# Kernel optimization log

Measured on AMD Instinct MI355X. Metric: run time of the kernel, lower is better.

Reference implementation:

```python
import jax, jax.numpy as jnp
import numpy as np

D_MODEL = 2048
N_HEADS = 32
N_KV_HEADS = 8
HEAD_DIM = D_MODEL // N_HEADS  # 64
N_REP = N_HEADS // N_KV_HEADS  # 4
SCALE = HEAD_DIM ** -0.5


def _rope_tables(seq_len):
    inv_freq = 1.0 / (10000.0 ** (jnp.arange(0, HEAD_DIM, 2, dtype=jnp.float32) / HEAD_DIM))
    t = jnp.arange(seq_len, dtype=jnp.float32)
    freqs = jnp.outer(t, inv_freq)  # [S, HEAD_DIM/2]
    return jnp.cos(freqs), jnp.sin(freqs)


def _apply_rope(x, cos, sin):
    # x: [b, h, s, d]; interleaved even/odd rotation, matching torch stack+flatten
    x_r, x_i = x[..., ::2], x[..., 1::2]
    out_r = x_r * cos - x_i * sin
    out_i = x_r * sin + x_i * cos
    out = jnp.stack([out_r, out_i], axis=-1)  # [b,h,s,d/2,2]
    return out.reshape(x.shape)


def setup_inputs() -> dict:
    key = jax.random.key(0)
    ks = jax.random.split(key, 5)
    bs, seq_len = 2, 2048
    std = D_MODEL ** -0.5
    x = jax.random.normal(ks[0], (bs, seq_len, D_MODEL), dtype=jnp.float32)
    wq = jax.random.normal(ks[1], (N_HEADS * HEAD_DIM, D_MODEL), dtype=jnp.float32) * std
    wk = jax.random.normal(ks[2], (N_KV_HEADS * HEAD_DIM, D_MODEL), dtype=jnp.float32) * std
    wv = jax.random.normal(ks[3], (N_KV_HEADS * HEAD_DIM, D_MODEL), dtype=jnp.float32) * std
    wo = jax.random.normal(ks[4], (D_MODEL, N_HEADS * HEAD_DIM), dtype=jnp.float32) * std
    return {"x": x, "wq": wq, "wk": wk, "wv": wv, "wo": wo}


def reference(x, wq, wk, wv, wo):
    bs, seq_len, _ = x.shape
    # fused-style QKV projections (nn.Linear: x @ W.T)
    q = (x @ wq.T).reshape(bs, seq_len, N_HEADS, HEAD_DIM).transpose(0, 2, 1, 3)
    k = (x @ wk.T).reshape(bs, seq_len, N_KV_HEADS, HEAD_DIM).transpose(0, 2, 1, 3)
    v = (x @ wv.T).reshape(bs, seq_len, N_KV_HEADS, HEAD_DIM).transpose(0, 2, 1, 3)
    cos, sin = _rope_tables(seq_len)  # [S, HEAD_DIM/2], broadcast over b,h
    q = _apply_rope(q, cos, sin)
    k = _apply_rope(k, cos, sin)
    # GQA: repeat KV heads to match Q heads
    k = jnp.repeat(k, N_REP, axis=1)  # [b, H, s, d]
    v = jnp.repeat(v, N_REP, axis=1)
    attn = jnp.einsum('bhqd,bhkd->bhqk', q, k) * SCALE
    causal = jnp.triu(jnp.ones((seq_len, seq_len), dtype=bool), k=1)
    attn = jnp.where(causal, -jnp.inf, attn)
    attn = jax.nn.softmax(attn, axis=-1)
    out = jnp.einsum('bhqk,bhkd->bhqd', attn, v)
    out = out.transpose(0, 2, 1, 3).reshape(bs, seq_len, D_MODEL)
    return out @ wo.T
```

## Files before the change

kernel.cpp:

```cpp
#include <hip/hip_runtime.h>

#define SEQ    2048
#define DM     2048
#define QKVN   3072
#define VTR    64

typedef short s16x8 __attribute__((ext_vector_type(8)));
typedef float f32x4 __attribute__((ext_vector_type(4)));
typedef float f32x16 __attribute__((ext_vector_type(16)));
typedef unsigned u32x4 __attribute__((ext_vector_type(4)));
typedef unsigned short us;

#define MFMA(a,b,c)   __builtin_amdgcn_mfma_f32_16x16x32_bf16((a),(b),(c),0,0,0)
#define MFMA32(a,b,c) __builtin_amdgcn_mfma_f32_32x32x16_bf16((a),(b),(c),0,0,0)

__device__ __forceinline__ float bf2f(us u) {
    unsigned v = ((unsigned)u) << 16;
    return __builtin_bit_cast(float, v);
}
__device__ __forceinline__ us f2bf(float f) {
    unsigned u = __builtin_bit_cast(unsigned, f);
    u += 0x7FFFu + ((u >> 16) & 1u);
    return (us)(u >> 16);
}
__device__ __forceinline__ unsigned cvtpk(float lo, float hi) {
    unsigned r;
    asm("v_cvt_pk_bf16_f32 %0, %1, %2" : "=v"(r) : "v"(lo), "v"(hi));
    return r;
}
__device__ __forceinline__ void glds16(const us* g, us* l) {
    __builtin_amdgcn_global_load_lds((__attribute__((address_space(1))) void*)g,
                                     (__attribute__((address_space(3))) void*)l, 16, 0, 0);
}

__global__ __launch_bounds__(256) void cvt_all(const float* __restrict__ x,
                                               const float* __restrict__ wq,
                                               const float* __restrict__ wk,
                                               const float* __restrict__ wv,
                                               const float* __restrict__ wo,
                                               us* __restrict__ xb,
                                               us* __restrict__ wdst) {
    int i = (blockIdx.x * blockDim.x + threadIdx.x) * 2;
    const float* src;
    int off;
    if (i < 2097152)      { src = x;  off = 0; }
    else {
        int j = i - 2097152;
        if (j < 1048576)      { src = wq; off = 2097152; }
        else if (j < 1310720) { src = wk; off = 2097152 + 1048576; }
        else if (j < 1572864) { src = wv; off = 2097152 + 1310720; }
        else                  { src = wo; off = 2097152 + 1572864; }
    }
    const int base = i - off;
    float4 v0 = ((const float4*)src)[base];
    float4 v1 = ((const float4*)src)[base + 1];
    s16x8 o;
    o[0] = (short)f2bf(v0.x); o[1] = (short)f2bf(v0.y);
    o[2] = (short)f2bf(v0.z); o[3] = (short)f2bf(v0.w);
    o[4] = (short)f2bf(v1.x); o[5] = (short)f2bf(v1.y);
    o[6] = (short)f2bf(v1.z); o[7] = (short)f2bf(v1.w);
    us* d = (i < 2097152) ? xb : wdst;
    const int di = (i < 2097152) ? i : i - 2097152;
    *(s16x8*)(d + di * 4) = o;
}

template <typename OutT, bool ROPE>
__global__ __launch_bounds__(512) void gemm_bt2(const us* __restrict__ A, const us* __restrict__ W,
                                                OutT* __restrict__ C, us* __restrict__ vt,
                                                int M, int N, int K) {
    __shared__ us lA[2][2][128 * 64];
    __shared__ us lB[2][2][128 * 64];
    const int tid = threadIdx.x, lane = tid & 63, wave = tid >> 6;
    const int quad = lane >> 4, lr = lane & 15;
    const int mh = wave >> 2;
    const int wnx = wave & 3;
    const int bh = wnx >> 1, br0 = (wnx & 1) * 64;
    const int m0 = blockIdx.x * 256, n0 = blockIdx.y * 256;

    const int srow = tid >> 3;
    const int scol = ((tid & 7) ^ (srow & 7)) * 8;
    const int sdst = srow * 64 + (tid & 7) * 8;

    const us* gA = A + (size_t)m0 * K;
    const us* gB = W + (size_t)n0 * K;

    auto stageH = [&](int s) {
        const int t = s >> 2, ty = s & 3, par = t & 1;
        const us* src;
        us* dst;
        if (ty < 2) { src = gA + (size_t)(ty * 128) * K;       dst = &lA[par][ty][0]; }
        else        { src = gB + (size_t)((ty - 2) * 128) * K; dst = &lB[par][ty - 2][0]; }
        src += t * 64;
        glds16(src + (size_t)srow * K + scol,        dst + sdst);
        glds16(src + (size_t)(srow + 64) * K + scol, dst + sdst + 64 * 64);
    };

    const int rsw = (lr & 7) << 3;
    auto rdA = [&](int par, int kk, int i) {
        return *(const s16x8*)&lA[par][mh][(i * 16 + lr) * 64 + ((kk * 32 + quad * 8) ^ rsw)];
    };
    auto rdB = [&](int par, int kk, int j) {
        return *(const s16x8*)&lB[par][bh][(br0 + j * 16 + lr) * 64 + ((kk * 32 + quad * 8) ^ rsw)];
    };

    f32x4 acc[8][4] = {};
    const int NT = K / 64;

    stageH(0); stageH(1); stageH(2); stageH(3); stageH(4);
    asm volatile("s_waitcnt vmcnt(2)" ::: "memory");
    __builtin_amdgcn_s_barrier();

    s16x8 af[2][4], ag[2][4], bfr[2][2], bg[2][2];
    for (int t = 0; t < NT; ++t) {
        const int par = t & 1;
#pragma unroll
        for (int kk = 0; kk < 2; kk++) {
#pragma unroll
            for (int i = 0; i < 4; i++) af[kk][i] = rdA(par, kk, i);
#pragma unroll
            for (int j = 0; j < 2; j++) bfr[kk][j] = rdB(par, kk, j);
        }
        if (t + 1 < NT) stageH(4 * (t + 1) + 1);
        __builtin_amdgcn_s_barrier();
        asm volatile("s_waitcnt lgkmcnt(0)" ::: "memory");
        __builtin_amdgcn_s_setprio(1);
#pragma unroll
        for (int i = 0; i < 4; i++)
#pragma unroll
            for (int j = 0; j < 2; j++)
#pragma unroll
                for (int kk = 0; kk < 2; kk++)
                    acc[i][j] = MFMA(af[kk][i], bfr[kk][j], acc[i][j]);
        __builtin_amdgcn_s_setprio(0);
        __builtin_amdgcn_s_barrier();
#pragma unroll
        for (int kk = 0; kk < 2; kk++)
#pragma unroll
            for (int j = 0; j < 2; j++) bg[kk][j] = rdB(par, kk, 2 + j);
        if (t + 1 < NT) stageH(4 * (t + 1) + 2);
        __builtin_amdgcn_s_barrier();
        asm volatile("s_waitcnt lgkmcnt(0)" ::: "memory");
        __builtin_amdgcn_s_setprio(1);
#pragma unroll
        for (int i = 0; i < 4; i++)
#pragma unroll
            for (int j = 0; j < 2; j++)
#pragma unroll
                for (int kk = 0; kk < 2; kk++)
                    acc[i][2 + j] = MFMA(af[kk][i], bg[kk][j], acc[i][2 + j]);
        __builtin_amdgcn_s_setprio(0);
        __builtin_amdgcn_s_barrier();
#pragma unroll
        for (int kk = 0; kk < 2; kk++)
#pragma unroll
            for (int i = 0; i < 4; i++) ag[kk][i] = rdA(par, kk, 4 + i);
        if (t + 1 < NT) stageH(4 * (t + 1) + 3);
        __builtin_amdgcn_s_barrier();
        asm volatile("s_waitcnt lgkmcnt(0)" ::: "memory");
        __builtin_amdgcn_s_setprio(1);
#pragma unroll
        for (int i = 0; i < 4; i++)
#pragma unroll
            for (int j = 0; j < 2; j++)
#pragma unroll
                for (int kk = 0; kk < 2; kk++)
                    acc[4 + i][j] = MFMA(ag[kk][i], bfr[kk][j], acc[4 + i][j]);
        __builtin_amdgcn_s_setprio(0);
        __builtin_amdgcn_s_barrier();
        if (t + 2 < NT) stageH(4 * (t + 2));
        __builtin_amdgcn_s_setprio(1);
#pragma unroll
        for (int i = 0; i < 4; i++)
#pragma unroll
            for (int j = 0; j < 2; j++)
#pragma unroll
                for (int kk = 0; kk < 2; kk++)
                    acc[4 + i][2 + j] = MFMA(ag[kk][i], bg[kk][j], acc[4 + i][2 + j]);
        __builtin_amdgcn_s_setprio(0);
        if (t + 1 < NT) {
            if (t + 2 < NT) asm volatile("s_waitcnt vmcnt(2)" ::: "memory");
            else            asm volatile("s_waitcnt vmcnt(0)" ::: "memory");
            __builtin_amdgcn_s_barrier();
        }
    }

    const bool vblk = ROPE && (n0 >= 2560);
#pragma unroll
    for (int i = 0; i < 8; i++)
#pragma unroll
        for (int j = 0; j < 4; j++) {
            const int row0 = m0 + mh * 128 + i * 16 + quad * 4;
            const int col  = n0 + wnx * 64 + j * 16 + lr;
            if (vblk) {
                const int d = col - 2560;
                const int b = row0 >> 11, s = row0 & (SEQ - 1);
                ushort4 o4;
                o4.x = f2bf(acc[i][j][0]); o4.y = f2bf(acc[i][j][1]);
                o4.z = f2bf(acc[i][j][2]); o4.w = f2bf(acc[i][j][3]);
                *(ushort4*)(vt + ((size_t)b * 512 + d) * SEQ + s) = o4;
            } else {
#pragma unroll
                for (int r = 0; r < 4; r++) {
                    const int row = row0 + r;
                    float v = acc[i][j][r];
                    if (ROPE && n0 < 2560) {
                        int pair = (col >> 1) & 31;
                        float inv = exp2f((float)pair * (-13.2877124f / 32.0f));
                        float ang = (float)(row & (SEQ - 1)) * inv;
                        float c = __cosf(ang), sn = __sinf(ang);
                        float p = __shfl_xor(v, 1);
                        v = v * c + ((col & 1) ? p * sn : -p * sn);
                    }
                    if constexpr (sizeof(OutT) == 2)
                        C[(size_t)row * N + col] = f2bf(v);
                    else
                        C[(size_t)row * N + col] = v;
                }
            }
        }
}

template <typename OutT>
__global__ __launch_bounds__(512) void gemm_bt2n(const us* __restrict__ A, const us* __restrict__ W,
                                                 OutT* __restrict__ C, int M, int N, int K) {
    __shared__ us lA[2][2][128 * 64];
    __shared__ us lB[2][128 * 64];
    const int tid = threadIdx.x, lane = tid & 63, wave = tid >> 6;
    const int quad = lane >> 4, lr = lane & 15;
    const int mh = wave >> 2;
    const int wnx = wave & 3;
    const int m0 = blockIdx.x * 256, n0 = blockIdx.y * 128;

    const int srow = tid >> 3;
    const int scol = ((tid & 7) ^ (srow & 7)) * 8;
    const int sdst = srow * 64 + (tid & 7) * 8;

    const us* gA = A + (size_t)m0 * K;
    const us* gB = W + (size_t)n0 * K;

    auto stageH = [&](int t, int ty) {
        const int par = t & 1;
        const us* src;
        us* dst;
        if (ty < 2) { src = gA + (size_t)(ty * 128) * K; dst = &lA[par][ty][0]; }
        else        { src = gB;                           dst = &lB[par][0]; }
        src += t * 64;
        glds16(src + (size_t)srow * K + scol,        dst + sdst);
        glds16(src + (size_t)(srow + 64) * K + scol, dst + sdst + 64 * 64);
    };

    const int rsw = (lr & 7) << 3;
    auto rdA = [&](int par, int kk, int i) {
        return *(const s16x8*)&lA[par][mh][(i * 16 + lr) * 64 + ((kk * 32 + quad * 8) ^ rsw)];
    };
    auto rdB = [&](int par, int kk, int j) {
        return *(const s16x8*)&lB[par][(wnx * 32 + j * 16 + lr) * 64 + ((kk * 32 + quad * 8) ^ rsw)];
    };

    f32x4 acc[8][2] = {};
    const int NT = K / 64;

    stageH(0, 0); stageH(0, 1); stageH(0, 2); stageH(1, 0);
    asm volatile("s_waitcnt vmcnt(2)" ::: "memory");
    __builtin_amdgcn_s_barrier();

    s16x8 af[2][4], ag[2][4], bfr[2][2];
    for (int t = 0; t < NT; ++t) {
        const int par = t & 1;
#pragma unroll
        for (int kk = 0; kk < 2; kk++) {
#pragma unroll
            for (int i = 0; i < 4; i++) af[kk][i] = rdA(par, kk, i);
#pragma unroll
            for (int j = 0; j < 2; j++) bfr[kk][j] = rdB(par, kk, j);
        }
        if (t + 1 < NT) stageH(t + 1, 1);
        __builtin_amdgcn_s_barrier();
        asm volatile("s_waitcnt lgkmcnt(0)" ::: "memory");
        __builtin_amdgcn_s_setprio(1);
#pragma unroll
        for (int i = 0; i < 4; i++)
#pragma unroll
            for (int j = 0; j < 2; j++)
#pragma unroll
                for (int kk = 0; kk < 2; kk++)
                    acc[i][j] = MFMA(af[kk][i], bfr[kk][j], acc[i][j]);
        __builtin_amdgcn_s_setprio(0);
        __builtin_amdgcn_s_barrier();
#pragma unroll
        for (int kk = 0; kk < 2; kk++)
#pragma unroll
            for (int i = 0; i < 4; i++) ag[kk][i] = rdA(par, kk, 4 + i);
        if (t + 1 < NT) stageH(t + 1, 2);
        __builtin_amdgcn_s_barrier();
        asm volatile("s_waitcnt lgkmcnt(0)" ::: "memory");
        __builtin_amdgcn_s_setprio(1);
#pragma unroll
        for (int i = 0; i < 4; i++)
#pragma unroll
            for (int j = 0; j < 2; j++)
#pragma unroll
                for (int kk = 0; kk < 2; kk++)
                    acc[4 + i][j] = MFMA(ag[kk][i], bfr[kk][j], acc[4 + i][j]);
        __builtin_amdgcn_s_setprio(0);
        if (t + 2 < NT) stageH(t + 2, 0);
        if (t + 1 < NT) {
            if (t + 2 < NT) asm volatile("s_waitcnt vmcnt(2)" ::: "memory");
            else            asm volatile("s_waitcnt vmcnt(0)" ::: "memory");
            __builtin_amdgcn_s_barrier();
        }
    }

#pragma unroll
    for (int i = 0; i < 8; i++)
#pragma unroll
        for (int j = 0; j < 2; j++)
#pragma unroll
            for (int r = 0; r < 4; r++) {
                int row = m0 + mh * 128 + i * 16 + quad * 4 + r;
                int col = n0 + wnx * 32 + j * 16 + lr;
                if constexpr (sizeof(OutT) == 2)
                    C[(size_t)row * N + col] = f2bf(acc[i][j][r]);
                else
                    C[(size_t)row * N + col] = acc[i][j][r];
            }
}

__global__ __launch_bounds__(256, 2) void flash_attn(const us* __restrict__ qkv,
                                                     const us* __restrict__ vt,
                                                     us* __restrict__ o) {
    const int bh = blockIdx.y, b = bh >> 5, h = bh & 31, kvh = h >> 2;
    const int wave = threadIdx.x >> 6, lane = threadIdx.x & 63;
    const int half = lane >> 5, l5 = lane & 31;
    const int jb = ((int)blockIdx.x + (int)(blockIdx.y >> 3)) & 7;
    const int j = jb * 4 + wave;
    const int q00 = j * 32, q01 = (63 - j) * 32;
    const int kbm0 = j, kbm1 = 63 - j;
    const us* kbase = qkv + (size_t)b * SEQ * QKVN + 2048 + kvh * 64;
    const us* vb = vt + (size_t)(b * 8 + kvh) * VTR * SEQ;
    const float QS = 0.125f * 1.44269504f;

    s16x8 qf[2][4];
#pragma unroll
    for (int t = 0; t < 2; t++) {
        const int q0t = t ? q01 : q00;
        const us* qb = qkv + (size_t)(b * SEQ + q0t + l5) * QKVN + h * 64 + half * 8;
#pragma unroll
        for (int dc = 0; dc < 4; dc++) {
            qf[t][dc] = *(const s16x8*)(qb + dc * 16);
#pragma unroll
            for (int e = 0; e < 8; e++)
                qf[t][dc][e] = (short)f2bf(bf2f((us)qf[t][dc][e]) * QS);
        }
    }

    f32x16 oacc[2][2] = {};
    float lsum0 = 0.f, lsum1 = 0.f;

    s16x8 kf[4], vf[4];
    auto load_k = [&](int kb) {
        const us* kp = kbase + (size_t)(kb * 32 + l5) * QKVN + half * 8;
#pragma unroll
        for (int dc = 0; dc < 4; dc++) kf[dc] = *(const s16x8*)(kp + dc * 16);
    };
    auto load_v = [&](int kb) {
#pragma unroll
        for (int kc = 0; kc < 2; kc++)
#pragma unroll
            for (int dh = 0; dh < 2; dh++)
                vf[kc * 2 + dh] = *(const s16x8*)(vb + (size_t)(dh * 32 + l5) * SEQ +
                                                  kb * 32 + kc * 16 + half * 8);
    };
    load_k(0);
    load_v(0);

    auto tilepv = [&](int kb, int kbt, int q0t, f32x16& sc, float& ls,
                      f32x16& od0, f32x16& od1) {
        float p[16];
        if (kb == kbt) {
#pragma unroll
            for (int r = 0; r < 16; r++) {
                int key = kb * 32 + (r & 3) + 8 * (r >> 2) + 4 * half;
                float s = (key > q0t + l5) ? -1e30f : sc[r];
                p[r] = exp2f(s);
                ls += p[r];
            }
        } else {
#pragma unroll
            for (int r = 0; r < 16; r++) { p[r] = exp2f(sc[r]); ls += p[r]; }
        }
        unsigned c01 = cvtpk(p[0], p[1]),   c23 = cvtpk(p[2], p[3]);
        unsigned c45 = cvtpk(p[4], p[5]),   c67 = cvtpk(p[6], p[7]);
        unsigned c89 = cvtpk(p[8], p[9]),   cab = cvtpk(p[10], p[11]);
        unsigned ccd = cvtpk(p[12], p[13]), cef = cvtpk(p[14], p[15]);
        asm("v_permlane32_swap_b32 %0, %1" : "+v"(c01), "+v"(c45));
        asm("v_permlane32_swap_b32 %0, %1" : "+v"(c23), "+v"(c67));
        asm("v_permlane32_swap_b32 %0, %1" : "+v"(c89), "+v"(ccd));
        asm("v_permlane32_swap_b32 %0, %1" : "+v"(cab), "+v"(cef));
        u32x4 w0, w1;
        w0[0] = c01; w0[1] = c23; w0[2] = c45; w0[3] = c67;
        w1[0] = c89; w1[1] = cab; w1[2] = ccd; w1[3] = cef;
        s16x8 fa0 = __builtin_bit_cast(s16x8, w0);
        s16x8 fa1 = __builtin_bit_cast(s16x8, w1);
        od0 = MFMA32(fa0, vf[0], od0);
        od0 = MFMA32(fa1, vf[2], od0);
        od1 = MFMA32(fa0, vf[1], od1);
        od1 = MFMA32(fa1, vf[3], od1);
    };

    for (int kb = 0; kb <= kbm1; kb++) {
        const bool a0 = (kb <= kbm0);
        f32x16 s0 = {}, s1 = {};
        if (a0) {
#pragma unroll
            for (int dc = 0; dc < 4; dc++) s0 = MFMA32(kf[dc], qf[0][dc], s0);
        }
#pragma unroll
        for (int dc = 0; dc < 4; dc++) s1 = MFMA32(kf[dc], qf[1][dc], s1);
        if (kb < kbm1) load_k(kb + 1);
        if (a0) tilepv(kb, kbm0, q00, s0, lsum0, oacc[0][0], oacc[0][1]);
        tilepv(kb, kbm1, q01, s1, lsum1, oacc[1][0], oacc[1][1]);
        if (kb < kbm1) load_v(kb + 1);
    }

#pragma unroll
    for (int t = 0; t < 2; t++) {
        const float lsel = t ? lsum1 : lsum0;
        const int q0t = t ? q01 : q00;
        const float lf = lsel + __shfl_xor(lsel, 32);
#pragma unroll
        for (int r = 0; r < 16; r++) {
            const int qrow = (r & 3) + 8 * (r >> 2) + 4 * half;
            const float li = 1.0f / __shfl(lf, qrow);
#pragma unroll
            for (int dh = 0; dh < 2; dh++) {
                const float v = (t ? oacc[1][dh][r] : oacc[0][dh][r]) * li;
                o[(size_t)(b * SEQ + q0t + qrow) * DM + h * 64 + dh * 32 + l5] = f2bf(v);
            }
        }
    }
}

extern "C" void kernel_launch(void* const* d_in, const int* in_sizes, int n_in,
                              void* d_out, int out_size, void* d_ws, size_t ws_size,
                              hipStream_t stream) {
    const float* x  = (const float*)d_in[0];
    const float* wq = (const float*)d_in[1];
    const float* wk = (const float*)d_in[2];
    const float* wv = (const float*)d_in[3];
    const float* wo = (const float*)d_in[4];
    float* out = (float*)d_out;

    char* ws = (char*)d_ws;
    const size_t MB = 1024 * 1024;
    us* xb     = (us*)(ws + 0 * MB);
    us* abuf   = (us*)(ws + 0 * MB);
    us* wqkvb  = (us*)(ws + 16 * MB);
    us* wob    = (us*)(ws + 28 * MB);
    us* qkvbuf = (us*)(ws + 36 * MB);
    us* vtbuf  = (us*)(ws + 60 * MB);

    dim3 blk(256);
    cvt_all<<<dim3(9216), blk, 0, stream>>>(x, wq, wk, wv, wo, xb, wqkvb);

    gemm_bt2<us, true><<<dim3(16, 12), dim3(512), 0, stream>>>(xb, wqkvb, qkvbuf, vtbuf,
                                                               4096, 3072, 2048);
    flash_attn<<<dim3(8, 64), blk, 0, stream>>>(qkvbuf, vtbuf, abuf);
    gemm_bt2n<float><<<dim3(16, 16), dim3(512), 0, stream>>>(abuf, wob, out, 4096, 2048, 2048);
}
```

Measured before the change: 330.5 us.

## Give each attention wave a single query tile, balancing causal work across waves

Previously each wave handled two paired query tiles (j and 63-j), sharing K/V loads across both. Now each wave handles one 32-row query tile, and the four waves of a block take tiles x, 31-x, 32+x and 63-x so the block's total causal work stays balanced. The grid doubles to 16x64 blocks and register use per wave drops, with the launch-bounds occupancy hint removed. The trade-off is that each K/V block is loaded once per query tile instead of being reused across two, and waves within a block now have unequal loop lengths.

Result: slower. 356.5 us (+7.9%).

```diff
diff --git a/kernel.cpp b/kernel.cpp
--- a/kernel.cpp
+++ b/kernel.cpp
@@ -326,36 +326,34 @@
             }
 }
 
-__global__ __launch_bounds__(256, 2) void flash_attn(const us* __restrict__ qkv,
-                                                     const us* __restrict__ vt,
-                                                     us* __restrict__ o) {
+__global__ __launch_bounds__(256) void flash_attn(const us* __restrict__ qkv,
+                                                  const us* __restrict__ vt,
+                                                  us* __restrict__ o) {
     const int bh = blockIdx.y, b = bh >> 5, h = bh & 31, kvh = h >> 2;
     const int wave = threadIdx.x >> 6, lane = threadIdx.x & 63;
     const int half = lane >> 5, l5 = lane & 31;
-    const int jb = ((int)blockIdx.x + (int)(blockIdx.y >> 3)) & 7;
-    const int j = jb * 4 + wave;
-    const int q00 = j * 32, q01 = (63 - j) * 32;
-    const int kbm0 = j, kbm1 = 63 - j;
+    const int x = ((int)blockIdx.x + (int)(blockIdx.y >> 2)) & 15;
+    const int j = (wave < 2) ? ((wave == 0) ? x : 31 - x)
+                             : ((wave == 2) ? 32 + x : 63 - x);
+    const int q0 = j * 32;
     const us* kbase = qkv + (size_t)b * SEQ * QKVN + 2048 + kvh * 64;
     const us* vb = vt + (size_t)(b * 8 + kvh) * VTR * SEQ;
     const float QS = 0.125f * 1.44269504f;
 
-    s16x8 qf[2][4];
-#pragma unroll
-    for (int t = 0; t < 2; t++) {
-        const int q0t = t ? q01 : q00;
-        const us* qb = qkv + (size_t)(b * SEQ + q0t + l5) * QKVN + h * 64 + half * 8;
+    s16x8 qf[4];
+    {
+        const us* qb = qkv + (size_t)(b * SEQ + q0 + l5) * QKVN + h * 64 + half * 8;
 #pragma unroll
         for (int dc = 0; dc < 4; dc++) {
-            qf[t][dc] = *(const s16x8*)(qb + dc * 16);
+            qf[dc] = *(const s16x8*)(qb + dc * 16);
 #pragma unroll
             for (int e = 0; e < 8; e++)
-                qf[t][dc][e] = (short)f2bf(bf2f((us)qf[t][dc][e]) * QS);
-        }
-    }
-
-    f32x16 oacc[2][2] = {};
-    float lsum0 = 0.f, lsum1 = 0.f;
+                qf[dc][e] = (short)f2bf(bf2f((us)qf[dc][e]) * QS);
+        }
+    }
+
+    f32x16 oacc0 = {}, oacc1 = {};
+    float lsum = 0.f;
 
     s16x8 kf[4], vf[4];
     auto load_k = [&](int kb) {
@@ -374,20 +372,23 @@
     load_k(0);
     load_v(0);
 
-    auto tilepv = [&](int kb, int kbt, int q0t, f32x16& sc, float& ls,
-                      f32x16& od0, f32x16& od1) {
+    for (int kb = 0; kb <= j; kb++) {
+        f32x16 sc = {};
+#pragma unroll
+        for (int dc = 0; dc < 4; dc++) sc = MFMA32(kf[dc], qf[dc], sc);
+        if (kb < j) load_k(kb + 1);
         float p[16];
-        if (kb == kbt) {
+        if (kb == j) {
 #pragma unroll
             for (int r = 0; r < 16; r++) {
                 int key = kb * 32 + (r & 3) + 8 * (r >> 2) + 4 * half;
-                float s = (key > q0t + l5) ? -1e30f : sc[r];
+                float s = (key > q0 + l5) ? -1e30f : sc[r];
                 p[r] = exp2f(s);
-                ls += p[r];
+                lsum += p[r];
             }
         } else {
 #pragma unroll
-            for (int r = 0; r < 16; r++) { p[r] = exp2f(sc[r]); ls += p[r]; }
+            for (int r = 0; r < 16; r++) { p[r] = exp2f(sc[r]); lsum += p[r]; }
         }
         unsigned c01 = cvtpk(p[0], p[1]),   c23 = cvtpk(p[2], p[3]);
         unsigned c45 = cvtpk(p[4], p[5]),   c67 = cvtpk(p[6], p[7]);
@@ -402,42 +403,20 @@
         w1[0] = c89; w1[1] = cab; w1[2] = ccd; w1[3] = cef;
         s16x8 fa0 = __builtin_bit_cast(s16x8, w0);
         s16x8 fa1 = __builtin_bit_cast(s16x8, w1);
-        od0 = MFMA32(fa0, vf[0], od0);
-        od0 = MFMA32(fa1, vf[2], od0);
-        od1 = MFMA32(fa0, vf[1], od1);
-        od1 = MFMA32(fa1, vf[3], od1);
-    };
-
-    for (int kb = 0; kb <= kbm1; kb++) {
-        const bool a0 = (kb <= kbm0);
-        f32x16 s0 = {}, s1 = {};
-        if (a0) {
-#pragma unroll
-            for (int dc = 0; dc < 4; dc++) s0 = MFMA32(kf[dc], qf[0][dc], s0);
-        }
-#pragma unroll
-        for (int dc = 0; dc < 4; dc++) s1 = MFMA32(kf[dc], qf[1][dc], s1);
-        if (kb < kbm1) load_k(kb + 1);
-        if (a0) tilepv(kb, kbm0, q00, s0, lsum0, oacc[0][0], oacc[0][1]);
-        tilepv(kb, kbm1, q01, s1, lsum1, oacc[1][0], oacc[1][1]);
-        if (kb < kbm1) load_v(kb + 1);
-    }
-
-#pragma unroll
-    for (int t = 0; t < 2; t++) {
-        const float lsel = t ? lsum1 : lsum0;
-        const int q0t = t ? q01 : q00;
-        const float lf = lsel + __shfl_xor(lsel, 32);
-#pragma unroll
-        for (int r = 0; r < 16; r++) {
-            const int qrow = (r & 3) + 8 * (r >> 2) + 4 * half;
-            const float li = 1.0f / __shfl(lf, qrow);
-#pragma unroll
-            for (int dh = 0; dh < 2; dh++) {
-                const float v = (t ? oacc[1][dh][r] : oacc[0][dh][r]) * li;
-                o[(size_t)(b * SEQ + q0t + qrow) * DM + h * 64 + dh * 32 + l5] = f2bf(v);
-            }
-        }
+        oacc0 = MFMA32(fa0, vf[0], oacc0);
+        oacc0 = MFMA32(fa1, vf[2], oacc0);
+        oacc1 = MFMA32(fa0, vf[1], oacc1);
+        oacc1 = MFMA32(fa1, vf[3], oacc1);
+        if (kb < j) load_v(kb + 1);
+    }
+
+    const float lf = lsum + __shfl_xor(lsum, 32);
+#pragma unroll
+    for (int r = 0; r < 16; r++) {
+        const int qrow = (r & 3) + 8 * (r >> 2) + 4 * half;
+        const float li = 1.0f / __shfl(lf, qrow);
+        o[(size_t)(b * SEQ + q0 + qrow) * DM + h * 64 + l5] = f2bf(oacc0[r] * li);
+        o[(size_t)(b * SEQ + q0 + qrow) * DM + h * 64 + 32 + l5] = f2bf(oacc1[r] * li);
     }
 }
 
@@ -465,6 +444,6 @@
 
     gemm_bt2<us, true><<<dim3(16, 12), dim3(512), 0, stream>>>(xb, wqkvb, qkvbuf, vtbuf,
                                                                4096, 3072, 2048);
-    flash_attn<<<dim3(8, 64), blk, 0, stream>>>(qkvbuf, vtbuf, abuf);
+    flash_attn<<<dim3(16, 64), blk, 0, stream>>>(qkvbuf, vtbuf, abuf);
     gemm_bt2n<float><<<dim3(16, 16), dim3(512), 0, stream>>>(abuf, wob, out, 4096, 2048, 2048);
 }
```
